# Kernel tuning notes

Hardware: AMD Instinct MI355X
Metric: run time of the kernel (lower is better)

The kernel has to match this reference:

```python
import jax, jax.numpy as jnp
import numpy as np

B, N_PER_GRAPH = 16, 512          # uniform graphs -> to_dense_batch is a reshape
N_TOKENS = B * N_PER_GRAPH
M = 32                            # neighbors per node
D_MODEL, D_EDGE, H = 256, 128, 8


def _layernorm(x, g, b, eps=1e-5):
    m = jnp.mean(x, axis=-1, keepdims=True)
    v = jnp.mean((x - m) ** 2, axis=-1, keepdims=True)
    return (x - m) * jax.lax.rsqrt(v + eps) * g + b


def _frame_ops():
    # 2^3 = 8 sign-flip operations, matches FrameAveraging.create_ops
    d = jnp.array([-1.0, 1.0], dtype=jnp.float32)
    g = jnp.meshgrid(d, d, d, indexing='ij')
    return jnp.stack(g, axis=-1).reshape(8, 3)


def _forward(token_embs, geo_feats, edge_feats, neighbor_indices, neighbor_masks,
             ln_qkv_g, ln_qkv_b, W_qkv, b_qkv, ln_e_g, ln_e_b, W_qkv_e, b_qkv_e,
             w_attn, w_edge, W_gate, b_gate, W_fc1, b_fc1, ln_h_g, ln_h_b,
             W_fc2, b_fc2, W_fa, b_fa):
    n = token_embs.shape[0]
    d_head = D_MODEL // H
    de_head = D_EDGE // H
    # qkv transformation
    qkv = _layernorm(token_embs, ln_qkv_g, ln_qkv_b) @ W_qkv + b_qkv
    q, k, v = [a.reshape(n, H, d_head) for a in jnp.split(qkv, 3, axis=-1)]
    qkve = _layernorm(edge_feats, ln_e_g, ln_e_b) @ W_qkv_e + b_qkv_e
    qe, ve = [a.reshape(n, M, H, de_head) for a in jnp.split(qkve, 2, axis=-1)]
    gate = jax.nn.sigmoid(token_embs @ W_gate + b_gate)            # [n,1]
    # GAT-style MLP attention over gathered neighbors
    message = q[:, None] + k[neighbor_indices]                     # [n,M,H,d]
    attn = jnp.einsum('nmhd,d->nmh', message, w_attn) \
         + jnp.einsum('nmhe,e->nmh', qe, w_edge)
    attn = jnp.where(neighbor_masks[..., None], attn, -1e9)
    attn = jax.nn.softmax(jnp.transpose(attn, (0, 2, 1)), axis=-1)  # [n,H,M]
    # context aggregation
    v_n = v[neighbor_indices]                                      # [n,M,H,d]
    scalar_ctx = jnp.einsum('nhm,nmhd->nhd', attn, v_n).reshape(n, -1)
    edge_ctx = jnp.einsum('nhm,nmhd->nhd', attn, ve).reshape(n, -1)
    hcat = jnp.concatenate([scalar_ctx, edge_ctx], axis=-1)
    hmid = _layernorm(jax.nn.gelu(hcat @ W_fc1 + b_fc1, approximate=False), ln_h_g, ln_h_b)
    scalar_out = hmid @ W_fc2 + b_fc2 + token_embs
    # geometric branch with frame averaging (n_heads > 1 path)
    Xb = geo_feats.reshape(B, N_PER_GRAPH, 3)                      # dense batch, full mask
    center = Xb.mean(axis=1)                                       # [B,3]
    Xc = Xb - center[:, None]
    C = jax.lax.stop_gradient(jnp.einsum('bni,bnj->bij', Xc, Xc))  # backward=False -> detach
    _, V = jnp.linalg.eigh(C)                                      # symmetric, UPLO irrelevant
    ops = _frame_ops()
    F_ops = jax.lax.stop_gradient(ops[None, :, None, :] * V[:, None])  # [B,8,3,3]
    h_fr = jnp.einsum('bpj,boji->bopi', Xc, F_ops)                 # [B,8,N,3]
    geo_f = jnp.transpose(h_fr, (1, 0, 2, 3)).reshape(8, n, 3)     # frame-major, node order b*N+p
    geo_neigh = geo_f[:, neighbor_indices]                         # [8,n,M,3]
    geo_ctx = jnp.einsum('nhm,fnmd->fnhd', attn, geo_neigh)        # [8,n,H,3]
    agg = jax.nn.silu(jnp.einsum('fnhd,h->fnd', geo_ctx, W_fa) + b_fa)  # W_frame_agg
    geo_b = jnp.transpose(agg, (1, 0, 2)).reshape(B, N_PER_GRAPH, 8, 3)
    geo_b = jnp.transpose(geo_b, (0, 2, 1, 3))                     # [B,8,N,3]
    inv = jnp.einsum('boij,bopj->bopi', F_ops, geo_b).mean(axis=1) + center[:, None]
    geo_context = inv.reshape(n, 3)
    geo_out = geo_context * gate + geo_feats * (1.0 - gate)
    return scalar_out, geo_out


def setup_inputs() -> dict:
    key = jax.random.key(0)
    ks = jax.random.split(key, 16)
    r = lambda k, shape, s=0.02: (jax.random.normal(k, shape) * s).astype(jnp.float32)
    token_embs = jax.random.normal(ks[0], (N_TOKENS, D_MODEL), dtype=jnp.float32)
    geo_feats = jax.random.normal(ks[1], (N_TOKENS, 3), dtype=jnp.float32)
    edge_feats = jax.random.normal(ks[2], (N_TOKENS, M, D_EDGE), dtype=jnp.float32)
    base = (jnp.arange(N_TOKENS) // N_PER_GRAPH) * N_PER_GRAPH
    neighbor_indices = base[:, None] + jax.random.randint(ks[3], (N_TOKENS, M), 0, N_PER_GRAPH)
    batch_idx = jnp.arange(N_TOKENS) // N_PER_GRAPH
    neighbor_masks = jax.random.uniform(ks[4], (N_TOKENS, M)) < 0.9
    d_head, de_head = D_MODEL // H, D_EDGE // H
    return dict(
        token_embs=token_embs, geo_feats=geo_feats, edge_feats=edge_feats,
        neighbor_indices=neighbor_indices, batch_idx=batch_idx, neighbor_masks=neighbor_masks,
        ln_qkv_g=jnp.ones(D_MODEL), ln_qkv_b=jnp.zeros(D_MODEL),
        W_qkv=r(ks[5], (D_MODEL, 3 * D_MODEL)), b_qkv=jnp.zeros(3 * D_MODEL),
        ln_e_g=jnp.ones(D_EDGE), ln_e_b=jnp.zeros(D_EDGE),
        W_qkv_e=r(ks[6], (D_EDGE, 2 * D_EDGE)), b_qkv_e=jnp.zeros(2 * D_EDGE),
        w_attn=r(ks[7], (d_head,), 0.1), w_edge=r(ks[8], (de_head,), 0.1),
        W_gate=jnp.zeros((D_MODEL, 1)), b_gate=jnp.ones((1,)),   # _init_params
        W_fc1=r(ks[9], (D_MODEL + D_EDGE, D_MODEL)), b_fc1=jnp.zeros(D_MODEL),
        ln_h_g=jnp.ones(D_MODEL), ln_h_b=jnp.zeros(D_MODEL),
        W_fc2=r(ks[10], (D_MODEL, D_MODEL)), b_fc2=jnp.zeros(D_MODEL),
        W_fa=r(ks[11], (H,), 0.3), b_fa=jnp.zeros((1,)),
    )


def reference(token_embs, geo_feats, edge_feats, neighbor_indices, batch_idx, neighbor_masks,
              ln_qkv_g, ln_qkv_b, W_qkv, b_qkv, ln_e_g, ln_e_b, W_qkv_e, b_qkv_e,
              w_attn, w_edge, W_gate, b_gate, W_fc1, b_fc1, ln_h_g, ln_h_b,
              W_fc2, b_fc2, W_fa, b_fa):
    # batch_idx is uniform (arange // N_PER_GRAPH); dense batching handled by reshape
    return _forward(token_embs, geo_feats, edge_feats, neighbor_indices, neighbor_masks,
                    ln_qkv_g, ln_qkv_b, W_qkv, b_qkv, ln_e_g, ln_e_b, W_qkv_e, b_qkv_e,
                    w_attn, w_edge, W_gate, b_gate, W_fc1, b_fc1, ln_h_g, ln_h_b,
                    W_fc2, b_fc2, W_fa, b_fa)
```

## Files before the change

kernel.cpp:

```cpp
#include <hip/hip_runtime.h>
#include <math.h>

#define NTOK 8192
#define NPG  512
#define MNEI 32
#define DM   256
#define DE   128
#define NH   8

#define OFF_WV    0u
#define OFF_WQAK  65536u
#define OFF_BCAT  69632u
#define OFF_WEF   69904u
#define OFF_BEF   70928u
#define OFF_FLAG  70936u
#define OFF_QA    70944u
#define OFF_KA    136480u
#define OFF_GATE  202016u
#define OFF_VW    210208u
#define OFF_PROJ  2307360u
#define OFF_VMAT  2331936u
#define OFF_CEN   2332080u
#define OFF_HCAT  2332128u

#define OUT_GEO_OFF 2097152

__device__ __forceinline__ void fma4x4(const float4 a, const float4 w, float4* acc) {
    acc[0].x += a.x*w.x; acc[0].y += a.x*w.y; acc[0].z += a.x*w.z; acc[0].w += a.x*w.w;
    acc[1].x += a.y*w.x; acc[1].y += a.y*w.y; acc[1].z += a.y*w.z; acc[1].w += a.y*w.w;
    acc[2].x += a.z*w.x; acc[2].y += a.z*w.y; acc[2].z += a.z*w.z; acc[2].w += a.z*w.w;
    acc[3].x += a.w*w.x; acc[3].y += a.w*w.y; acc[3].z += a.w*w.z; acc[3].w += a.w*w.w;
}

__device__ __forceinline__ float dot4(const float4 a, const float4 b) {
    return a.x*b.x + a.y*b.y + a.z*b.z + a.w*b.w;
}

__global__ __launch_bounds__(256) void k_fold(
    const float* __restrict__ Wqkv, const float* __restrict__ bqkv,
    const float* __restrict__ Wqkve, const float* __restrict__ bqkve,
    const float* __restrict__ w_attn, const float* __restrict__ w_edge,
    const float* __restrict__ lneg, const float* __restrict__ lneb,
    const int* __restrict__ maskp, float* __restrict__ ws)
{
    int t = threadIdx.x;
    if (blockIdx.x == 0) {
        __shared__ int sbad, sflt;
        if (t == 0) { sbad = 0; sflt = 0; }
        __syncthreads();
        int bad = 0, flt = 0;
        for (int i = 0; i < 256; i++) {
            unsigned int w = (unsigned int)maskp[i*256 + t];
            if (w > 1u) bad = 1;
            if (w == 0x3F800000u) flt = 1;
        }
        if (bad) atomicOr(&sbad, 1);
        if (flt) atomicOr(&sflt, 1);
        __syncthreads();
        if (t == 0) {
            int f = sflt ? 2 : (sbad ? 1 : 0);
            ((int*)(ws + OFF_FLAG))[0] = f;
        }
        return;
    }
    int gid = (blockIdx.x - 1) * 256 + t;
    if (gid < 65536) {
        int k = gid >> 8, c = gid & 255;
        ws[OFF_WV + gid] = Wqkv[k*768 + 512 + c];
    } else if (gid < 69632) {
        int idx = gid - 65536;
        int c = idx >> 8, k = idx & 255;
        int h = c & 7; int off = (c < 8) ? 0 : 256;
        float s = 0.f;
        for (int d = 0; d < 32; d++) s += Wqkv[k*768 + off + h*32 + d] * w_attn[d];
        ws[OFF_WQAK + idx] = s;
    } else if (gid < 69632 + 272) {
        int c = gid - 69632;
        float val;
        if (c < 8) {
            int h = c;
            float s = 0.f;
            for (int d = 0; d < 32; d++) s += bqkv[h*32 + d] * w_attn[d];
            for (int e = 0; e < 16; e++) s += bqkve[h*16 + e] * w_edge[e];
            for (int r = 0; r < 128; r++) {
                float wef = 0.f;
                for (int e = 0; e < 16; e++) wef += Wqkve[r*256 + h*16 + e] * w_edge[e];
                s += lneb[r] * wef;
            }
            val = s;
        } else if (c < 16) {
            int h = c & 7;
            float s = 0.f;
            for (int d = 0; d < 32; d++) s += bqkv[256 + h*32 + d] * w_attn[d];
            val = s;
        } else {
            val = bqkv[512 + (c - 16)];
        }
        ws[OFF_BCAT + c] = val;
    } else if (gid < 69904 + 1024) {
        int i = gid - 69904;
        int h = i >> 7, r = i & 127;
        float s = 0.f;
        for (int e = 0; e < 16; e++) s += Wqkve[r*256 + h*16 + e] * w_edge[e];
        ws[OFF_WEF + i] = s * lneg[r];
    }
}

__global__ __launch_bounds__(256) void k_tokprep(
    const float* __restrict__ tok, const float* __restrict__ ln_g,
    const float* __restrict__ ln_b, const float* __restrict__ Wgate,
    const float* __restrict__ bgate, float* __restrict__ ws)
{
    __shared__ __align__(16) float sln[256 * 12];
    int t = threadIdx.x;
    int tok0 = blockIdx.x * 8;

    #pragma unroll
    for (int q = 0; q < 8; q++)
        sln[t*12 + q] = tok[(size_t)(tok0 + q) * 256 + t];
    __syncthreads();

    int wave = t >> 6, lane = t & 63;
    for (int rr = 0; rr < 2; rr++) {
        int tt = wave * 2 + rr;
        float s = 0.f, gdot = 0.f;
        float xs[4];
        #pragma unroll
        for (int q = 0; q < 4; q++) {
            int k = lane + 64*q;
            float x = sln[k*12 + tt];
            xs[q] = x; s += x; gdot += x * Wgate[k];
        }
        for (int m = 32; m >= 1; m >>= 1) { s += __shfl_xor(s,m,64); gdot += __shfl_xor(gdot,m,64); }
        float mu = s * (1.0f/256.0f);
        float vs = 0.f;
        #pragma unroll
        for (int q = 0; q < 4; q++) { float d = xs[q]-mu; vs += d*d; }
        for (int m = 32; m >= 1; m >>= 1) vs += __shfl_xor(vs,m,64);
        float rinv = rsqrtf(vs*(1.0f/256.0f)+1e-5f);
        #pragma unroll
        for (int q = 0; q < 4; q++) {
            int k = lane + 64*q;
            sln[k*12 + tt] = (xs[q]-mu)*rinv*ln_g[k] + ln_b[k];
        }
        if (lane == 0) ws[OFF_GATE + tok0 + tt] = 1.0f/(1.0f+expf(-(gdot + bgate[0])));
    }
    __syncthreads();

    if (t < 128) {
        int i = t >> 6, j = t & 63;
        const float* Wc = ws + OFF_WV + 4*j;
        float4 acc[4];
        acc[0] = acc[1] = acc[2] = acc[3] = make_float4(0.f,0.f,0.f,0.f);
        #pragma unroll 8
        for (int k = 0; k < 256; k++) {
            float4 a4 = *(const float4*)&sln[k*12 + 4*i];
            float4 w4 = *(const float4*)&Wc[(size_t)k*256];
            fma4x4(a4, w4, acc);
        }
        float4 b4 = *(const float4*)&ws[OFF_BCAT + 16 + 4*j];
        #pragma unroll
        for (int ti = 0; ti < 4; ti++) {
            int n = tok0 + 4*i + ti;
            float4 v = acc[ti];
            v.x += b4.x; v.y += b4.y; v.z += b4.z; v.w += b4.w;
            *(float4*)&ws[OFF_VW + (size_t)n*256 + 4*j] = v;
        }
    } else {
        int wave3 = (t >> 6) - 2;
        int col = t & 15, tp = (t & 63) >> 4;
        int tokn = wave3*4 + tp;
        const float* wq = ws + OFF_WQAK + col*256;
        float acc = 0.f;
        #pragma unroll 8
        for (int k4 = 0; k4 < 64; k4++) {
            float4 w4 = *(const float4*)&wq[4*k4];
            acc += w4.x * sln[(4*k4+0)*12 + tokn]
                 + w4.y * sln[(4*k4+1)*12 + tokn]
                 + w4.z * sln[(4*k4+2)*12 + tokn]
                 + w4.w * sln[(4*k4+3)*12 + tokn];
        }
        acc += ws[OFF_BCAT + col];
        int n = tok0 + tokn;
        if (col < 8) ws[OFF_QA + n*8 + col] = acc;
        else         ws[OFF_KA + n*8 + (col - 8)] = acc;
    }
}

__global__ __launch_bounds__(256) void k_geo(const float* __restrict__ geo, float* __restrict__ ws)
{
    __shared__ float sred[4 * 9];
    __shared__ float sres[9];
    __shared__ float sV[9];
    int t = threadIdx.x, g = blockIdx.x;
    int wave = t >> 6, lane = t & 63;
    const float* gp = geo + (size_t)g * NPG * 3;

    float x0[2], y0[2], z0[2];
    float sx = 0.f, sy = 0.f, sz = 0.f;
    for (int i = 0; i < 2; i++) {
        int p = t + 256 * i;
        x0[i] = gp[p*3 + 0]; y0[i] = gp[p*3 + 1]; z0[i] = gp[p*3 + 2];
        sx += x0[i]; sy += y0[i]; sz += z0[i];
    }
    {
        float vals[3] = {sx, sy, sz};
        for (int q = 0; q < 3; q++) {
            float v = vals[q];
            for (int m = 32; m >= 1; m >>= 1) v += __shfl_xor(v, m, 64);
            if (lane == 0) sred[wave*9 + q] = v;
        }
    }
    __syncthreads();
    if (t < 3) {
        float s = 0.f;
        for (int w = 0; w < 4; w++) s += sred[w*9 + t];
        sres[t] = s * (1.0f / 512.0f);
    }
    __syncthreads();
    float cx = sres[0], cy = sres[1], cz = sres[2];

    float c6[6] = {0.f, 0.f, 0.f, 0.f, 0.f, 0.f};
    for (int i = 0; i < 2; i++) {
        float dx = x0[i] - cx, dy = y0[i] - cy, dz = z0[i] - cz;
        c6[0] += dx*dx; c6[1] += dx*dy; c6[2] += dx*dz;
        c6[3] += dy*dy; c6[4] += dy*dz; c6[5] += dz*dz;
    }
    for (int q = 0; q < 6; q++) {
        float v = c6[q];
        for (int m = 32; m >= 1; m >>= 1) v += __shfl_xor(v, m, 64);
        if (lane == 0) sred[wave*9 + q] = v;
    }
    __syncthreads();
    if (t < 6) {
        float s = 0.f;
        for (int w = 0; w < 4; w++) s += sred[w*9 + t];
        sres[t] = s;
    }
    __syncthreads();

    if (t == 0) {
        double a[3][3];
        a[0][0] = sres[0]; a[0][1] = a[1][0] = sres[1]; a[0][2] = a[2][0] = sres[2];
        a[1][1] = sres[3]; a[1][2] = a[2][1] = sres[4]; a[2][2] = sres[5];
        double v[3][3] = {{1,0,0},{0,1,0},{0,0,1}};
        const int ps[3] = {0, 0, 1}, qs[3] = {1, 2, 2};
        for (int sweep = 0; sweep < 10; sweep++) {
            for (int pi = 0; pi < 3; pi++) {
                int p = ps[pi], q = qs[pi];
                double apq = a[p][q];
                if (fabs(apq) < 1e-300) continue;
                double theta = (a[q][q] - a[p][p]) / (2.0 * apq);
                double tt = ((theta >= 0.0) ? 1.0 : -1.0) / (fabs(theta) + sqrt(theta*theta + 1.0));
                double c = 1.0 / sqrt(tt*tt + 1.0), s = tt * c;
                int k = 3 - p - q;
                double app = a[p][p], aqq = a[q][q], akp = a[k][p], akq = a[k][q];
                a[p][p] = app - tt * apq;
                a[q][q] = aqq + tt * apq;
                a[p][q] = 0.0; a[q][p] = 0.0;
                a[k][p] = c*akp - s*akq; a[p][k] = a[k][p];
                a[k][q] = s*akp + c*akq; a[q][k] = a[k][q];
                for (int kk = 0; kk < 3; kk++) {
                    double vp = v[kk][p], vq = v[kk][q];
                    v[kk][p] = c*vp - s*vq;
                    v[kk][q] = s*vp + c*vq;
                }
            }
        }
        for (int r = 0; r < 3; r++)
            for (int c2 = 0; c2 < 3; c2++) {
                float fv = (float)v[r][c2];
                sV[r*3 + c2] = fv;
                ws[OFF_VMAT + g*9 + r*3 + c2] = fv;
            }
        ws[OFF_CEN + g*3 + 0] = cx;
        ws[OFF_CEN + g*3 + 1] = cy;
        ws[OFF_CEN + g*3 + 2] = cz;
    }
    __syncthreads();

    for (int i = 0; i < 2; i++) {
        int p = t + 256 * i;
        float dx = x0[i] - cx, dy = y0[i] - cy, dz = z0[i] - cz;
        for (int c = 0; c < 3; c++) {
            float pr = dx * sV[0*3 + c] + dy * sV[1*3 + c] + dz * sV[2*3 + c];
            ws[OFF_PROJ + (size_t)(g*NPG + p)*3 + c] = pr;
        }
    }
}

__global__ __launch_bounds__(256) void k_attn(
    const float* __restrict__ edge, const int* __restrict__ nbr,
    const void* __restrict__ maskp,
    const float* __restrict__ lneg, const float* __restrict__ lneb,
    const float* __restrict__ bqkve, const float* __restrict__ Wqkve,
    const float* __restrict__ Wfa, const float* __restrict__ bfa,
    const float* __restrict__ geo, float* __restrict__ ws, float* __restrict__ out)
{
    __shared__ __align__(16) float se[32 * 132];
    __shared__ __align__(16) float uSWE[8 * 132];
    __shared__ __align__(16) float sattn[8 * 36];
    __shared__ float srinv[32];
    __shared__ int   snbr[32];
    __shared__ float sg3[4];

    int t = threadIdx.x;
    int n = blockIdx.x;
    int g = n >> 9;
    int flag = ((const int*)(ws + OFF_FLAG))[0];

    int m = t >> 3, sub = t & 7;

    const float4* xp = (const float4*)(edge + (size_t)n * 4096 + m*128 + sub*16);
    float4 x0 = xp[0], x1 = xp[1], x2 = xp[2], x3 = xp[3];
    {
        int idx = t * 4;
        int h = idx >> 7, r = idx & 127;
        int s2 = r >> 4, c = r & 15;
        *(float4*)&uSWE[s2*132 + h*16 + c] = *(const float4*)&ws[OFF_WEF + idx];
    }
    if (t < 32) snbr[t] = nbr[n*32 + t];
    __syncthreads();

    {
        float s = x0.x+x0.y+x0.z+x0.w + x1.x+x1.y+x1.z+x1.w
                + x2.x+x2.y+x2.z+x2.w + x3.x+x3.y+x3.z+x3.w;
        for (int mm = 4; mm >= 1; mm >>= 1) s += __shfl_xor(s, mm, 8);
        float mu = s * (1.0f / 128.0f);
        x0.x-=mu; x0.y-=mu; x0.z-=mu; x0.w-=mu;
        x1.x-=mu; x1.y-=mu; x1.z-=mu; x1.w-=mu;
        x2.x-=mu; x2.y-=mu; x2.z-=mu; x2.w-=mu;
        x3.x-=mu; x3.y-=mu; x3.z-=mu; x3.w-=mu;
        float vs = dot4(x0,x0) + dot4(x1,x1) + dot4(x2,x2) + dot4(x3,x3);
        for (int mm = 4; mm >= 1; mm >>= 1) vs += __shfl_xor(vs, mm, 8);
        float rinv = rsqrtf(vs * (1.0f / 128.0f) + 1e-5f);
        float4* sp = (float4*)&se[m*132 + sub*16];
        sp[0] = x0; sp[1] = x1; sp[2] = x2; sp[3] = x3;
        if (sub == 0) srinv[m] = rinv;

        float accl[8];
        const float* wb = &uSWE[sub*132];
        #pragma unroll
        for (int h = 0; h < 8; h++) {
            const float4* wp = (const float4*)(wb + h*16);
            accl[h] = dot4(x0,wp[0]) + dot4(x1,wp[1]) + dot4(x2,wp[2]) + dot4(x3,wp[3]);
        }
        #pragma unroll
        for (int st = 1; st < 8; st <<= 1) {
            #pragma unroll
            for (int h = 0; h < 8; h++) accl[h] += __shfl_xor(accl[h], st, 8);
        }
        float myacc = accl[0];
        #pragma unroll
        for (int h = 1; h < 8; h++) myacc = (sub == h) ? accl[h] : myacc;

        int mv;
        if (flag == 1)      mv = (int)((const unsigned char*)maskp)[n*32 + m];
        else if (flag == 2) mv = (((const float*)maskp)[n*32 + m] != 0.0f) ? 1 : 0;
        else                mv = ((const int*)maskp)[n*32 + m];

        float lg = myacc * rinv
                 + ws[OFF_QA + n*8 + sub]
                 + ws[OFF_KA + (size_t)snbr[m]*8 + sub];
        if (!mv) lg = -1e9f;
        sattn[sub*36 + m] = lg;
    }
    __syncthreads();

    {
        int h = t >> 5, m2 = t & 31;
        float x = sattn[h*36 + m2];
        float mx = x;
        for (int mm = 16; mm >= 1; mm >>= 1) mx = fmaxf(mx, __shfl_xor(mx, mm, 32));
        float e = expf(x - mx);
        float sum = e;
        for (int mm = 16; mm >= 1; mm >>= 1) sum += __shfl_xor(sum, mm, 32);
        sattn[h*36 + m2] = e / sum;
    }
    __syncthreads();

    float* sew = uSWE;

    int wave = t >> 6;
    if (wave == 0) {
        int c4 = t, h = c4 >> 3;
        const float* vw = ws + OFF_VW;
        float4 acc = make_float4(0.f,0.f,0.f,0.f);
        #pragma unroll 4
        for (int mi = 0; mi < 32; mi++) {
            float a = sattn[h*36 + mi];
            int row = snbr[mi];
            float4 v4 = *(const float4*)&vw[(size_t)row*256 + 4*c4];
            acc.x += a*v4.x; acc.y += a*v4.y; acc.z += a*v4.z; acc.w += a*v4.w;
        }
        *(float4*)&ws[OFF_HCAT + (size_t)n*384 + 4*c4] = acc;
    } else if (wave == 1) {
        int lm = t - 64;
        if (lm < 32) {
            float wmv = 0.f;
            #pragma unroll
            for (int h2 = 0; h2 < 8; h2++) wmv += Wfa[h2] * sattn[h2*36 + lm];
            int row = snbr[lm];
            const float* pp = ws + OFF_PROJ + (size_t)row*3;
            float q0 = wmv * pp[0], q1 = wmv * pp[1], q2 = wmv * pp[2];
            for (int st = 16; st >= 1; st >>= 1) {
                q0 += __shfl_xor(q0, st, 32);
                q1 += __shfl_xor(q1, st, 32);
                q2 += __shfl_xor(q2, st, 32);
            }
            if (lm < 3) {
                float sd = (lm == 0) ? q0 : (lm == 1) ? q1 : q2;
                float bb = bfa[0];
                float p1 = sd + bb, p2 = -sd + bb;
                float s1v = p1 / (1.0f + expf(-p1));
                float s2v = p2 / (1.0f + expf(-p2));
                sg3[lm] = 0.5f * (s1v - s2v);
            }
        }
    } else {
        int rq = t & 31, hb = (t >> 5) & 3;
        float4 e1 = make_float4(0.f,0.f,0.f,0.f);
        float4 e2 = make_float4(0.f,0.f,0.f,0.f);
        #pragma unroll 4
        for (int mi = 0; mi < 32; mi++) {
            float ri = srinv[mi];
            float a1 = sattn[hb*36 + mi] * ri;
            float a2 = sattn[(hb+4)*36 + mi] * ri;
            float4 x4 = *(const float4*)&se[mi*132 + 4*rq];
            e1.x += a1*x4.x; e1.y += a1*x4.y; e1.z += a1*x4.z; e1.w += a1*x4.w;
            e2.x += a2*x4.x; e2.y += a2*x4.y; e2.z += a2*x4.z; e2.w += a2*x4.w;
        }
        float4 g4 = *(const float4*)&lneg[4*rq];
        float4 b4 = *(const float4*)&lneb[4*rq];
        float4 o1, o2;
        o1.x = g4.x*e1.x + b4.x; o1.y = g4.y*e1.y + b4.y;
        o1.z = g4.z*e1.z + b4.z; o1.w = g4.w*e1.w + b4.w;
        o2.x = g4.x*e2.x + b4.x; o2.y = g4.y*e2.y + b4.y;
        o2.z = g4.z*e2.z + b4.z; o2.w = g4.w*e2.w + b4.w;
        *(float4*)&sew[hb*132 + 4*rq]     = o1;
        *(float4*)&sew[(hb+4)*132 + 4*rq] = o2;
    }
    __syncthreads();

    float* sec = se;
    {
        int col4 = t & 31, rgrp = t >> 5;
        int h2 = col4 >> 2;
        const float* wqb = Wqkve + 128 + 4*col4;
        float4 accE = make_float4(0.f,0.f,0.f,0.f);
        #pragma unroll 4
        for (int ri = 0; ri < 16; ri++) {
            int r = rgrp*16 + ri;
            float sv = sew[h2*132 + r];
            float4 w4 = *(const float4*)&wqb[(size_t)r*256];
            accE.x += sv*w4.x; accE.y += sv*w4.y; accE.z += sv*w4.z; accE.w += sv*w4.w;
        }
        *(float4*)&sec[rgrp*128 + 4*col4] = accE;
    }
    __syncthreads();

    if (t < 128) {
        float ec = bqkve[128 + t];
        #pragma unroll
        for (int g2 = 0; g2 < 8; g2++) ec += sec[g2*128 + t];
        ws[OFF_HCAT + (size_t)n*384 + 256 + t] = ec;
    }
    if (t < 3) {
        const float* Vm = ws + OFF_VMAT + g*9;
        float gc = Vm[t*3+0]*sg3[0] + Vm[t*3+1]*sg3[1] + Vm[t*3+2]*sg3[2] + ws[OFF_CEN + g*3 + t];
        float gt = ws[OFF_GATE + n];
        out[OUT_GEO_OFF + (size_t)n*3 + t] = gc * gt + geo[(size_t)n*3 + t] * (1.0f - gt);
    }
}

__global__ __launch_bounds__(256) void k_mlp(
    const float* __restrict__ tok, const float* __restrict__ Wfc1,
    const float* __restrict__ bfc1, const float* __restrict__ lnhg,
    const float* __restrict__ lnhb, const float* __restrict__ Wfc2,
    const float* __restrict__ bfc2, const float* __restrict__ ws,
    float* __restrict__ out)
{
    __shared__ __align__(16) float A[384 * 12];
    __shared__ __align__(16) float R[128 * 16];
    int t = threadIdx.x;
    int tok0 = blockIdx.x * 8;
    int i2 = (t >> 6) & 1, kh = t >> 7, j = t & 63;
    const float* hc = ws + OFF_HCAT;

    #pragma unroll
    for (int q = 0; q < 12; q++) {
        int idx = q*256 + t;
        int tt = idx / 384;
        int k  = idx - tt*384;
        A[k*12 + tt] = hc[(size_t)tok0*384 + idx];
    }
    __syncthreads();

    float4 acc1[4];
    acc1[0] = acc1[1] = acc1[2] = acc1[3] = make_float4(0.f,0.f,0.f,0.f);
    {
        const float* wp = Wfc1 + 4*j;
        int kbase = kh * 192;
        #pragma unroll 8
        for (int kk = 0; kk < 192; kk++) {
            int k = kbase + kk;
            float4 a4 = *(const float4*)&A[k*12 + 4*i2];
            float4 w4 = *(const float4*)&wp[(size_t)k*256];
            fma4x4(a4, w4, acc1);
        }
    }
    if (kh == 1) {
        int rowid = t - 128;
        #pragma unroll
        for (int ti = 0; ti < 4; ti++) *(float4*)&R[rowid*16 + ti*4] = acc1[ti];
    }
    __syncthreads();

    float h[4][4];
    if (kh == 0) {
        float4 b4 = *(const float4*)&bfc1[4*j];
        #pragma unroll
        for (int ti = 0; ti < 4; ti++) {
            float4 p = *(const float4*)&R[t*16 + ti*4];
            float xv[4] = {acc1[ti].x + p.x + b4.x, acc1[ti].y + p.y + b4.y,
                           acc1[ti].z + p.z + b4.z, acc1[ti].w + p.w + b4.w};
            #pragma unroll
            for (int c = 0; c < 4; c++) {
                float x = xv[c];
                h[ti][c] = 0.5f * x * (1.0f + erff(x * 0.70710678118654752f));
            }
        }
        float s[4], qv[4];
        #pragma unroll
        for (int ti = 0; ti < 4; ti++) {
            s[ti]  = h[ti][0] + h[ti][1] + h[ti][2] + h[ti][3];
            qv[ti] = h[ti][0]*h[ti][0] + h[ti][1]*h[ti][1] + h[ti][2]*h[ti][2] + h[ti][3]*h[ti][3];
        }
        for (int m = 32; m >= 1; m >>= 1)
            #pragma unroll
            for (int ti = 0; ti < 4; ti++) {
                s[ti]  += __shfl_xor(s[ti], m, 64);
                qv[ti] += __shfl_xor(qv[ti], m, 64);
            }
        float4 g4 = *(const float4*)&lnhg[4*j];
        float4 b42 = *(const float4*)&lnhb[4*j];
        float gg[4] = {g4.x, g4.y, g4.z, g4.w};
        float bb[4] = {b42.x, b42.y, b42.z, b42.w};
        #pragma unroll
        for (int ti = 0; ti < 4; ti++) {
            float mu = s[ti] * (1.0f/256.0f);
            float var = qv[ti] * (1.0f/256.0f) - mu*mu;
            float rinv = rsqrtf(var + 1e-5f);
            #pragma unroll
            for (int c = 0; c < 4; c++) {
                float hn = (h[ti][c] - mu) * rinv * gg[c] + bb[c];
                A[(4*j + c)*12 + 4*i2 + ti] = hn;
            }
        }
    }
    __syncthreads();

    float4 acc2[4];
    acc2[0] = acc2[1] = acc2[2] = acc2[3] = make_float4(0.f,0.f,0.f,0.f);
    {
        const float* wp = Wfc2 + 4*j;
        int kbase = kh * 128;
        #pragma unroll 8
        for (int kk = 0; kk < 128; kk++) {
            int k = kbase + kk;
            float4 a4 = *(const float4*)&A[k*12 + 4*i2];
            float4 w4 = *(const float4*)&wp[(size_t)k*256];
            fma4x4(a4, w4, acc2);
        }
    }
    if (kh == 1) {
        int rowid = t - 128;
        #pragma unroll
        for (int ti = 0; ti < 4; ti++) *(float4*)&R[rowid*16 + ti*4] = acc2[ti];
    }
    __syncthreads();

    if (kh == 0) {
        float4 b4 = *(const float4*)&bfc2[4*j];
        #pragma unroll
        for (int ti = 0; ti < 4; ti++) {
            float4 p = *(const float4*)&R[t*16 + ti*4];
            size_t o = (size_t)(tok0 + 4*i2 + ti) * 256 + 4*j;
            float4 r4 = *(const float4*)&tok[o];
            float4 v;
            v.x = acc2[ti].x + p.x + b4.x + r4.x;
            v.y = acc2[ti].y + p.y + b4.y + r4.y;
            v.z = acc2[ti].z + p.z + b4.z + r4.z;
            v.w = acc2[ti].w + p.w + b4.w + r4.w;
            *(float4*)&out[o] = v;
        }
    }
}

extern "C" void kernel_launch(void* const* d_in, const int* in_sizes, int n_in,
                              void* d_out, int out_size, void* d_ws, size_t ws_size,
                              hipStream_t stream) {
    (void)in_sizes; (void)n_in; (void)out_size; (void)ws_size;
    const float* tok   = (const float*)d_in[0];
    const float* geo   = (const float*)d_in[1];
    const float* edge  = (const float*)d_in[2];
    const int*   nbr   = (const int*)d_in[3];
    const void*  maskp = d_in[5];
    const float* ln_qkv_g = (const float*)d_in[6];
    const float* ln_qkv_b = (const float*)d_in[7];
    const float* Wqkv  = (const float*)d_in[8];
    const float* bqkv  = (const float*)d_in[9];
    const float* ln_e_g = (const float*)d_in[10];
    const float* ln_e_b = (const float*)d_in[11];
    const float* Wqkve = (const float*)d_in[12];
    const float* bqkve = (const float*)d_in[13];
    const float* w_attn = (const float*)d_in[14];
    const float* w_edge = (const float*)d_in[15];
    const float* Wgate = (const float*)d_in[16];
    const float* bgate = (const float*)d_in[17];
    const float* Wfc1  = (const float*)d_in[18];
    const float* bfc1  = (const float*)d_in[19];
    const float* lnhg  = (const float*)d_in[20];
    const float* lnhb  = (const float*)d_in[21];
    const float* Wfc2  = (const float*)d_in[22];
    const float* bfc2  = (const float*)d_in[23];
    const float* Wfa   = (const float*)d_in[24];
    const float* bfa   = (const float*)d_in[25];
    float* ws  = (float*)d_ws;
    float* out = (float*)d_out;

    k_fold<<<dim3(279), dim3(256), 0, stream>>>(Wqkv, bqkv, Wqkve, bqkve, w_attn, w_edge,
                                                ln_e_g, ln_e_b, (const int*)maskp, ws);
    k_tokprep<<<dim3(1024), dim3(256), 0, stream>>>(tok, ln_qkv_g, ln_qkv_b, Wgate, bgate, ws);
    k_geo<<<dim3(16), dim3(256), 0, stream>>>(geo, ws);
    k_attn<<<dim3(8192), dim3(256), 0, stream>>>(edge, nbr, maskp, ln_e_g, ln_e_b, bqkve,
                                                 Wqkve, Wfa, bfa, geo, ws, out);
    k_mlp<<<dim3(1024), dim3(256), 0, stream>>>(tok, Wfc1, bfc1, lnhg, lnhb, Wfc2, bfc2, ws, out);
}
```

Measured before the change: 393.3 us.

## Merge fold and geo prep kernels, read Wv directly, shuffle-reduce edge ctx

Folds the weight-folding kernel and the per-graph geometry (PCA frame) kernel into one 38-block prep kernel, which removes one launch. The V-weight copy into the workspace is dropped, and k_tokprep now reads Wqkv directly with all 256 threads computing V, two tokens each. The q/k attention-logit projection in that kernel moves to the first 128 threads. In k_attn the edge-context reduction now uses 8-lane shuffles instead of a shared-memory pass plus a barrier, which removes one __syncthreads per token. The cost is strided 768-wide global reads of Wqkv and a serialized Jacobi solve that sits in the same launch as the fold work.

Result: slower. 423.2 us (+7.6%).

```diff
diff --git a/kernel.cpp b/kernel.cpp
--- a/kernel.cpp
+++ b/kernel.cpp
@@ -12,7 +12,6 @@
 #define OFF_WQAK  65536u
 #define OFF_BCAT  69632u
 #define OFF_WEF   69904u
-#define OFF_BEF   70928u
 #define OFF_FLAG  70936u
 #define OFF_QA    70944u
 #define OFF_KA    136480u
@@ -36,15 +35,18 @@
     return a.x*b.x + a.y*b.y + a.z*b.z + a.w*b.w;
 }
 
-__global__ __launch_bounds__(256) void k_fold(
+__global__ __launch_bounds__(256) void k_pre(
     const float* __restrict__ Wqkv, const float* __restrict__ bqkv,
     const float* __restrict__ Wqkve, const float* __restrict__ bqkve,
     const float* __restrict__ w_attn, const float* __restrict__ w_edge,
     const float* __restrict__ lneg, const float* __restrict__ lneb,
-    const int* __restrict__ maskp, float* __restrict__ ws)
+    const int* __restrict__ maskp, const float* __restrict__ geo,
+    float* __restrict__ ws)
 {
     int t = threadIdx.x;
-    if (blockIdx.x == 0) {
+    int b = blockIdx.x;
+
+    if (b == 0) {
         __shared__ int sbad, sflt;
         if (t == 0) { sbad = 0; sflt = 0; }
         __syncthreads();
@@ -63,53 +65,153 @@
         }
         return;
     }
-    int gid = (blockIdx.x - 1) * 256 + t;
-    if (gid < 65536) {
-        int k = gid >> 8, c = gid & 255;
-        ws[OFF_WV + gid] = Wqkv[k*768 + 512 + c];
-    } else if (gid < 69632) {
-        int idx = gid - 65536;
-        int c = idx >> 8, k = idx & 255;
+    if (b == 1) {
+        int h = t >> 5, l = t & 31;
+        float p = 0.f;
+        for (int q = 0; q < 4; q++) {
+            int r = l + 32*q;
+            float wef = 0.f;
+            for (int e = 0; e < 16; e++) wef += Wqkve[r*256 + h*16 + e] * w_edge[e];
+            p += lneb[r] * wef;
+        }
+        for (int m = 16; m >= 1; m >>= 1) p += __shfl_xor(p, m, 32);
+        if (l == 0) {
+            float s = p;
+            for (int d = 0; d < 32; d++) s += bqkv[h*32 + d] * w_attn[d];
+            for (int e = 0; e < 16; e++) s += bqkve[h*16 + e] * w_edge[e];
+            ws[OFF_BCAT + h] = s;
+        }
+        if (l == 1) {
+            float s = 0.f;
+            for (int d = 0; d < 32; d++) s += bqkv[256 + h*32 + d] * w_attn[d];
+            ws[OFF_BCAT + 8 + h] = s;
+        }
+        return;
+    }
+    if (b < 18) {
+        int c = b - 2, k = t;
         int h = c & 7; int off = (c < 8) ? 0 : 256;
         float s = 0.f;
         for (int d = 0; d < 32; d++) s += Wqkv[k*768 + off + h*32 + d] * w_attn[d];
-        ws[OFF_WQAK + idx] = s;
-    } else if (gid < 69632 + 272) {
-        int c = gid - 69632;
-        float val;
-        if (c < 8) {
-            int h = c;
-            float s = 0.f;
-            for (int d = 0; d < 32; d++) s += bqkv[h*32 + d] * w_attn[d];
-            for (int e = 0; e < 16; e++) s += bqkve[h*16 + e] * w_edge[e];
-            for (int r = 0; r < 128; r++) {
-                float wef = 0.f;
-                for (int e = 0; e < 16; e++) wef += Wqkve[r*256 + h*16 + e] * w_edge[e];
-                s += lneb[r] * wef;
-            }
-            val = s;
-        } else if (c < 16) {
-            int h = c & 7;
-            float s = 0.f;
-            for (int d = 0; d < 32; d++) s += bqkv[256 + h*32 + d] * w_attn[d];
-            val = s;
-        } else {
-            val = bqkv[512 + (c - 16)];
-        }
-        ws[OFF_BCAT + c] = val;
-    } else if (gid < 69904 + 1024) {
-        int i = gid - 69904;
+        ws[OFF_WQAK + c*256 + k] = s;
+        return;
+    }
+    if (b < 22) {
+        int i = (b - 18)*256 + t;
         int h = i >> 7, r = i & 127;
         float s = 0.f;
         for (int e = 0; e < 16; e++) s += Wqkve[r*256 + h*16 + e] * w_edge[e];
         ws[OFF_WEF + i] = s * lneg[r];
+        return;
+    }
+
+    {
+        __shared__ float sred[4 * 9];
+        __shared__ float sres[9];
+        __shared__ float sV[9];
+        int g = b - 22;
+        int wave = t >> 6, lane = t & 63;
+        const float* gp = geo + (size_t)g * NPG * 3;
+
+        float x0[2], y0[2], z0[2];
+        float sx = 0.f, sy = 0.f, sz = 0.f;
+        for (int i = 0; i < 2; i++) {
+            int p = t + 256 * i;
+            x0[i] = gp[p*3 + 0]; y0[i] = gp[p*3 + 1]; z0[i] = gp[p*3 + 2];
+            sx += x0[i]; sy += y0[i]; sz += z0[i];
+        }
+        {
+            float vals[3] = {sx, sy, sz};
+            for (int q = 0; q < 3; q++) {
+                float v = vals[q];
+                for (int m = 32; m >= 1; m >>= 1) v += __shfl_xor(v, m, 64);
+                if (lane == 0) sred[wave*9 + q] = v;
+            }
+        }
+        __syncthreads();
+        if (t < 3) {
+            float s = 0.f;
+            for (int w = 0; w < 4; w++) s += sred[w*9 + t];
+            sres[t] = s * (1.0f / 512.0f);
+        }
+        __syncthreads();
+        float cx = sres[0], cy = sres[1], cz = sres[2];
+
+        float c6[6] = {0.f, 0.f, 0.f, 0.f, 0.f, 0.f};
+        for (int i = 0; i < 2; i++) {
+            float dx = x0[i] - cx, dy = y0[i] - cy, dz = z0[i] - cz;
+            c6[0] += dx*dx; c6[1] += dx*dy; c6[2] += dx*dz;
+            c6[3] += dy*dy; c6[4] += dy*dz; c6[5] += dz*dz;
+        }
+        for (int q = 0; q < 6; q++) {
+            float v = c6[q];
+            for (int m = 32; m >= 1; m >>= 1) v += __shfl_xor(v, m, 64);
+            if (lane == 0) sred[wave*9 + q] = v;
+        }
+        __syncthreads();
+        if (t < 6) {
+            float s = 0.f;
+            for (int w = 0; w < 4; w++) s += sred[w*9 + t];
+            sres[t] = s;
+        }
+        __syncthreads();
+
+        if (t == 0) {
+            double a[3][3];
+            a[0][0] = sres[0]; a[0][1] = a[1][0] = sres[1]; a[0][2] = a[2][0] = sres[2];
+            a[1][1] = sres[3]; a[1][2] = a[2][1] = sres[4]; a[2][2] = sres[5];
+            double v[3][3] = {{1,0,0},{0,1,0},{0,0,1}};
+            const int ps[3] = {0, 0, 1}, qs[3] = {1, 2, 2};
+            for (int sweep = 0; sweep < 10; sweep++) {
+                for (int pi = 0; pi < 3; pi++) {
+                    int p = ps[pi], q = qs[pi];
+                    double apq = a[p][q];
+                    if (fabs(apq) < 1e-300) continue;
+                    double theta = (a[q][q] - a[p][p]) / (2.0 * apq);
+                    double tt = ((theta >= 0.0) ? 1.0 : -1.0) / (fabs(theta) + sqrt(theta*theta + 1.0));
+                    double c = 1.0 / sqrt(tt*tt + 1.0), s = tt * c;
+                    int k = 3 - p - q;
+                    double app = a[p][p], aqq = a[q][q], akp = a[k][p], akq = a[k][q];
+                    a[p][p] = app - tt * apq;
+                    a[q][q] = aqq + tt * apq;
+                    a[p][q] = 0.0; a[q][p] = 0.0;
+                    a[k][p] = c*akp - s*akq; a[p][k] = a[k][p];
+                    a[k][q] = s*akp + c*akq; a[q][k] = a[k][q];
+                    for (int kk = 0; kk < 3; kk++) {
+                        double vp = v[kk][p], vq = v[kk][q];
+                        v[kk][p] = c*vp - s*vq;
+                        v[kk][q] = s*vp + c*vq;
+                    }
+                }
+            }
+            for (int r = 0; r < 3; r++)
+                for (int c2 = 0; c2 < 3; c2++) {
+                    float fv = (float)v[r][c2];
+                    sV[r*3 + c2] = fv;
+                    ws[OFF_VMAT + g*9 + r*3 + c2] = fv;
+                }
+            ws[OFF_CEN + g*3 + 0] = cx;
+            ws[OFF_CEN + g*3 + 1] = cy;
+            ws[OFF_CEN + g*3 + 2] = cz;
+        }
+        __syncthreads();
+
+        for (int i = 0; i < 2; i++) {
+            int p = t + 256 * i;
+            float dx = x0[i] - cx, dy = y0[i] - cy, dz = z0[i] - cz;
+            for (int c = 0; c < 3; c++) {
+                float pr = dx * sV[0*3 + c] + dy * sV[1*3 + c] + dz * sV[2*3 + c];
+                ws[OFF_PROJ + (size_t)(g*NPG + p)*3 + c] = pr;
+            }
+        }
     }
 }
 
 __global__ __launch_bounds__(256) void k_tokprep(
     const float* __restrict__ tok, const float* __restrict__ ln_g,
     const float* __restrict__ ln_b, const float* __restrict__ Wgate,
-    const float* __restrict__ bgate, float* __restrict__ ws)
+    const float* __restrict__ bgate, const float* __restrict__ Wqkv,
+    const float* __restrict__ bqkv, float* __restrict__ ws)
 {
     __shared__ __align__(16) float sln[256 * 12];
     int t = threadIdx.x;
@@ -147,145 +249,43 @@
     }
     __syncthreads();
 
-    if (t < 128) {
+    {
         int i = t >> 6, j = t & 63;
-        const float* Wc = ws + OFF_WV + 4*j;
-        float4 acc[4];
-        acc[0] = acc[1] = acc[2] = acc[3] = make_float4(0.f,0.f,0.f,0.f);
+        const float* Wc = Wqkv + 512 + 4*j;
+        float4 acc0 = make_float4(0.f,0.f,0.f,0.f);
+        float4 acc1 = make_float4(0.f,0.f,0.f,0.f);
         #pragma unroll 8
         for (int k = 0; k < 256; k++) {
-            float4 a4 = *(const float4*)&sln[k*12 + 4*i];
-            float4 w4 = *(const float4*)&Wc[(size_t)k*256];
-            fma4x4(a4, w4, acc);
-        }
-        float4 b4 = *(const float4*)&ws[OFF_BCAT + 16 + 4*j];
-        #pragma unroll
-        for (int ti = 0; ti < 4; ti++) {
-            int n = tok0 + 4*i + ti;
-            float4 v = acc[ti];
-            v.x += b4.x; v.y += b4.y; v.z += b4.z; v.w += b4.w;
-            *(float4*)&ws[OFF_VW + (size_t)n*256 + 4*j] = v;
-        }
-    } else {
-        int wave3 = (t >> 6) - 2;
-        int col = t & 15, tp = (t & 63) >> 4;
-        int tokn = wave3*4 + tp;
+            float a0 = sln[k*12 + 2*i];
+            float a1 = sln[k*12 + 2*i + 1];
+            float4 w4 = *(const float4*)&Wc[(size_t)k*768];
+            acc0.x += a0*w4.x; acc0.y += a0*w4.y; acc0.z += a0*w4.z; acc0.w += a0*w4.w;
+            acc1.x += a1*w4.x; acc1.y += a1*w4.y; acc1.z += a1*w4.z; acc1.w += a1*w4.w;
+        }
+        float4 b4 = *(const float4*)&bqkv[512 + 4*j];
+        int n0 = tok0 + 2*i;
+        acc0.x += b4.x; acc0.y += b4.y; acc0.z += b4.z; acc0.w += b4.w;
+        acc1.x += b4.x; acc1.y += b4.y; acc1.z += b4.z; acc1.w += b4.w;
+        *(float4*)&ws[OFF_VW + (size_t)n0*256 + 4*j]     = acc0;
+        *(float4*)&ws[OFF_VW + (size_t)(n0+1)*256 + 4*j] = acc1;
+    }
+
+    if (t < 128) {
+        int col = t & 15, tp = t >> 4;
         const float* wq = ws + OFF_WQAK + col*256;
         float acc = 0.f;
         #pragma unroll 8
         for (int k4 = 0; k4 < 64; k4++) {
             float4 w4 = *(const float4*)&wq[4*k4];
-            acc += w4.x * sln[(4*k4+0)*12 + tokn]
-                 + w4.y * sln[(4*k4+1)*12 + tokn]
-                 + w4.z * sln[(4*k4+2)*12 + tokn]
-                 + w4.w * sln[(4*k4+3)*12 + tokn];
+            acc += w4.x * sln[(4*k4+0)*12 + tp]
+                 + w4.y * sln[(4*k4+1)*12 + tp]
+                 + w4.z * sln[(4*k4+2)*12 + tp]
+                 + w4.w * sln[(4*k4+3)*12 + tp];
         }
         acc += ws[OFF_BCAT + col];
-        int n = tok0 + tokn;
+        int n = tok0 + tp;
         if (col < 8) ws[OFF_QA + n*8 + col] = acc;
         else         ws[OFF_KA + n*8 + (col - 8)] = acc;
-    }
-}
-
-__global__ __launch_bounds__(256) void k_geo(const float* __restrict__ geo, float* __restrict__ ws)
-{
-    __shared__ float sred[4 * 9];
-    __shared__ float sres[9];
-    __shared__ float sV[9];
-    int t = threadIdx.x, g = blockIdx.x;
-    int wave = t >> 6, lane = t & 63;
-    const float* gp = geo + (size_t)g * NPG * 3;
-
-    float x0[2], y0[2], z0[2];
-    float sx = 0.f, sy = 0.f, sz = 0.f;
-    for (int i = 0; i < 2; i++) {
-        int p = t + 256 * i;
-        x0[i] = gp[p*3 + 0]; y0[i] = gp[p*3 + 1]; z0[i] = gp[p*3 + 2];
-        sx += x0[i]; sy += y0[i]; sz += z0[i];
-    }
-    {
-        float vals[3] = {sx, sy, sz};
-        for (int q = 0; q < 3; q++) {
-            float v = vals[q];
-            for (int m = 32; m >= 1; m >>= 1) v += __shfl_xor(v, m, 64);
-            if (lane == 0) sred[wave*9 + q] = v;
-        }
-    }
-    __syncthreads();
-    if (t < 3) {
-        float s = 0.f;
-        for (int w = 0; w < 4; w++) s += sred[w*9 + t];
-        sres[t] = s * (1.0f / 512.0f);
-    }
-    __syncthreads();
-    float cx = sres[0], cy = sres[1], cz = sres[2];
-
-    float c6[6] = {0.f, 0.f, 0.f, 0.f, 0.f, 0.f};
-    for (int i = 0; i < 2; i++) {
-        float dx = x0[i] - cx, dy = y0[i] - cy, dz = z0[i] - cz;
-        c6[0] += dx*dx; c6[1] += dx*dy; c6[2] += dx*dz;
-        c6[3] += dy*dy; c6[4] += dy*dz; c6[5] += dz*dz;
-    }
-    for (int q = 0; q < 6; q++) {
-        float v = c6[q];
-        for (int m = 32; m >= 1; m >>= 1) v += __shfl_xor(v, m, 64);
-        if (lane == 0) sred[wave*9 + q] = v;
-    }
-    __syncthreads();
-    if (t < 6) {
-        float s = 0.f;
-        for (int w = 0; w < 4; w++) s += sred[w*9 + t];
-        sres[t] = s;
-    }
-    __syncthreads();
-
-    if (t == 0) {
-        double a[3][3];
-        a[0][0] = sres[0]; a[0][1] = a[1][0] = sres[1]; a[0][2] = a[2][0] = sres[2];
-        a[1][1] = sres[3]; a[1][2] = a[2][1] = sres[4]; a[2][2] = sres[5];
-        double v[3][3] = {{1,0,0},{0,1,0},{0,0,1}};
-        const int ps[3] = {0, 0, 1}, qs[3] = {1, 2, 2};
-        for (int sweep = 0; sweep < 10; sweep++) {
-            for (int pi = 0; pi < 3; pi++) {
-                int p = ps[pi], q = qs[pi];
-                double apq = a[p][q];
-                if (fabs(apq) < 1e-300) continue;
-                double theta = (a[q][q] - a[p][p]) / (2.0 * apq);
-                double tt = ((theta >= 0.0) ? 1.0 : -1.0) / (fabs(theta) + sqrt(theta*theta + 1.0));
-                double c = 1.0 / sqrt(tt*tt + 1.0), s = tt * c;
-                int k = 3 - p - q;
-                double app = a[p][p], aqq = a[q][q], akp = a[k][p], akq = a[k][q];
-                a[p][p] = app - tt * apq;
-                a[q][q] = aqq + tt * apq;
-                a[p][q] = 0.0; a[q][p] = 0.0;
-                a[k][p] = c*akp - s*akq; a[p][k] = a[k][p];
-                a[k][q] = s*akp + c*akq; a[q][k] = a[k][q];
-                for (int kk = 0; kk < 3; kk++) {
-                    double vp = v[kk][p], vq = v[kk][q];
-                    v[kk][p] = c*vp - s*vq;
-                    v[kk][q] = s*vp + c*vq;
-                }
-            }
-        }
-        for (int r = 0; r < 3; r++)
-            for (int c2 = 0; c2 < 3; c2++) {
-                float fv = (float)v[r][c2];
-                sV[r*3 + c2] = fv;
-                ws[OFF_VMAT + g*9 + r*3 + c2] = fv;
-            }
-        ws[OFF_CEN + g*3 + 0] = cx;
-        ws[OFF_CEN + g*3 + 1] = cy;
-        ws[OFF_CEN + g*3 + 2] = cz;
-    }
-    __syncthreads();
-
-    for (int i = 0; i < 2; i++) {
-        int p = t + 256 * i;
-        float dx = x0[i] - cx, dy = y0[i] - cy, dz = z0[i] - cz;
-        for (int c = 0; c < 3; c++) {
-            float pr = dx * sV[0*3 + c] + dy * sV[1*3 + c] + dz * sV[2*3 + c];
-            ws[OFF_PROJ + (size_t)(g*NPG + p)*3 + c] = pr;
-        }
     }
 }
 
@@ -442,29 +442,32 @@
     }
     __syncthreads();
 
-    float* sec = se;
-    {
-        int col4 = t & 31, rgrp = t >> 5;
+    {
+        int col4 = t >> 3, ks = t & 7;
         int h2 = col4 >> 2;
         const float* wqb = Wqkve + 128 + 4*col4;
         float4 accE = make_float4(0.f,0.f,0.f,0.f);
         #pragma unroll 4
         for (int ri = 0; ri < 16; ri++) {
-            int r = rgrp*16 + ri;
+            int r = ri*8 + ks;
             float sv = sew[h2*132 + r];
             float4 w4 = *(const float4*)&wqb[(size_t)r*256];
             accE.x += sv*w4.x; accE.y += sv*w4.y; accE.z += sv*w4.z; accE.w += sv*w4.w;
         }
-        *(float4*)&sec[rgrp*128 + 4*col4] = accE;
-    }
-    __syncthreads();
-
-    if (t < 128) {
-        float ec = bqkve[128 + t];
-        #pragma unroll
-        for (int g2 = 0; g2 < 8; g2++) ec += sec[g2*128 + t];
-        ws[OFF_HCAT + (size_t)n*384 + 256 + t] = ec;
-    }
+        #pragma unroll
+        for (int st = 1; st < 8; st <<= 1) {
+            accE.x += __shfl_xor(accE.x, st, 8);
+            accE.y += __shfl_xor(accE.y, st, 8);
+            accE.z += __shfl_xor(accE.z, st, 8);
+            accE.w += __shfl_xor(accE.w, st, 8);
+        }
+        if (ks == 0) {
+            float4 b4 = *(const float4*)&bqkve[128 + 4*col4];
+            accE.x += b4.x; accE.y += b4.y; accE.z += b4.z; accE.w += b4.w;
+            *(float4*)&ws[OFF_HCAT + (size_t)n*384 + 256 + 4*col4] = accE;
+        }
+    }
+
     if (t < 3) {
         const float* Vm = ws + OFF_VMAT + g*9;
         float gc = Vm[t*3+0]*sg3[0] + Vm[t*3+1]*sg3[1] + Vm[t*3+2]*sg3[2] + ws[OFF_CEN + g*3 + t];
@@ -629,10 +632,10 @@
     float* ws  = (float*)d_ws;
     float* out = (float*)d_out;
 
-    k_fold<<<dim3(279), dim3(256), 0, stream>>>(Wqkv, bqkv, Wqkve, bqkve, w_attn, w_edge,
-                                                ln_e_g, ln_e_b, (const int*)maskp, ws);
-    k_tokprep<<<dim3(1024), dim3(256), 0, stream>>>(tok, ln_qkv_g, ln_qkv_b, Wgate, bgate, ws);
-    k_geo<<<dim3(16), dim3(256), 0, stream>>>(geo, ws);
+    k_pre<<<dim3(38), dim3(256), 0, stream>>>(Wqkv, bqkv, Wqkve, bqkve, w_attn, w_edge,
+                                              ln_e_g, ln_e_b, (const int*)maskp, geo, ws);
+    k_tokprep<<<dim3(1024), dim3(256), 0, stream>>>(tok, ln_qkv_g, ln_qkv_b, Wgate, bgate,
+                                                    Wqkv, bqkv, ws);
     k_attn<<<dim3(8192), dim3(256), 0, stream>>>(edge, nbr, maskp, ln_e_g, ln_e_b, bqkve,
                                                  Wqkve, Wfa, bfa, geo, ws, out);
     k_mlp<<<dim3(1024), dim3(256), 0, stream>>>(tok, Wfc1, bfc1, lnhg, lnhb, Wfc2, bfc2, ws, out);
```
